# Performance work log

Measured on AMD Instinct MI355X. Metric: run time of the kernel, lower is better.

Reference implementation:

```python
import jax, jax.numpy as jnp
import numpy as np

N, M, D = 32768, 8192, 256


def setup_inputs() -> dict:
    key = jax.random.key(0)
    kx, ky = jax.random.split(key)
    inputDataX = jax.random.normal(kx, (N, D), dtype=jnp.float32)
    targetDataY = jax.random.normal(ky, (M, D), dtype=jnp.float32)
    dualVariablePsi = jnp.zeros((M,), dtype=jnp.float32)
    return {"inputDataX": inputDataX, "targetDataY": targetDataY, "dualVariablePsi": dualVariablePsi}


def reference(inputDataX, targetDataY, dualVariablePsi):
    # cost[i,j] = 0.5 * ||x_i - y_j||^2, built GEMM-style as in the torch module
    sq_x = jnp.sum(inputDataX ** 2, axis=1, keepdims=True)          # [N, 1]
    sq_y = jnp.sum(targetDataY ** 2, axis=1)[None, :]               # [1, M]
    cross = inputDataX @ targetDataY.T                              # [N, M]
    cost = (sq_x + sq_y - 2.0 * cross) * 0.5
    row_min = jnp.min(cost - dualVariablePsi[None, :], axis=1)      # [N]
    n = inputDataX.shape[0]
    return jnp.sum(row_min) / n + jnp.mean(dualVariablePsi)
```

## Files before the change

### kernel.cpp

```cpp
#include <hip/hip_runtime.h>
#include <hip/hip_bf16.h>
#include <stdint.h>

#define NROWS 32768
#define MCOLS 8192
#define DDIM  256

#define BM 128
#define BN 64
#define NT (MCOLS/BN)
#define NWG (NROWS/BM)

typedef __attribute__((ext_vector_type(8))) int   int8v;
typedef __attribute__((ext_vector_type(4))) float f32x4;

__device__ __forceinline__ uint32_t pk4_fp8(float4 v) {
  int p = __builtin_amdgcn_cvt_pk_fp8_f32(v.x, v.y, 0, false);
  p = __builtin_amdgcn_cvt_pk_fp8_f32(v.z, v.w, p, true);
  return (uint32_t)p;
}
__device__ __forceinline__ f32x4 vmin4(f32x4 x, f32x4 y) {
  f32x4 r;
  r[0] = fminf(x[0], y[0]); r[1] = fminf(x[1], y[1]);
  r[2] = fminf(x[2], y[2]); r[3] = fminf(x[3], y[3]);
  return r;
}

__global__ void k_prep(const float* __restrict__ X, const float* __restrict__ Y,
                       const float* __restrict__ psi,
                       uint32_t* __restrict__ XqN, uint32_t* __restrict__ YqT,
                       float* __restrict__ xhalf, float* __restrict__ cbuf,
                       float* __restrict__ sum_accum)
{
  const int lane = threadIdx.x & 63;
  const int gw = (blockIdx.x * blockDim.x + threadIdx.x) >> 6;
  const int nw = (gridDim.x * blockDim.x) >> 6;
  for (int row = gw; row < NROWS + MCOLS; row += nw) {
    const bool isX = row < NROWS;
    const int r = isX ? row : row - NROWS;
    const float* src = isX ? (X + (size_t)row * DDIM) : (Y + (size_t)r * DDIM);
    float4 v = ((const float4*)src)[lane];
    const uint32_t pk = pk4_fp8(v);
    if (isX) {
      XqN[(size_t)row * 64 + lane] = pk ^ 0x80808080u;
    } else {
      const int idx = (r >> 4) * 1024 + (lane >> 5) * 512 + ((lane >> 3) & 3) * 128
                    + (r & 15) * 8 + (lane & 7);
      YqT[idx] = pk;
    }
    float s = v.x*v.x + v.y*v.y + v.z*v.z + v.w*v.w;
    #pragma unroll
    for (int m = 32; m >= 1; m >>= 1) s += __shfl_xor(s, m);
    if (lane == 0) {
      if (isX) xhalf[row] = 0.5f * s;
      else     cbuf[r] = 0.5f * s - psi[r];
    }
  }
  if (blockIdx.x == 0 && threadIdx.x == 0) sum_accum[0] = 0.0f;
}

#define LOADB(dst, cjv, t_) do {                                                \
    const char* _p = bBase + (size_t)(t_) * 16384;                              \
    dst[0] = *(const int8v*)(_p);                                               \
    dst[1] = *(const int8v*)(_p + 2048);                                        \
    cjv = cjPtr[(t_) * BN];                                                     \
  } while (0)

#define STEP(t_, CUR, cjv) do {                                                 \
    const f32x4 _ci = {cjv, cjv, cjv, cjv};                                     \
    f32x4 acc[4];                                                               \
    __builtin_amdgcn_s_setprio(1);                                              \
    _Pragma("unroll") for (int _m = 0; _m < 4; ++_m)                            \
      acc[_m] = __builtin_amdgcn_mfma_scale_f32_16x16x128_f8f6f4(               \
          a[_m][0], CUR[0], _ci, 0, 0, 0, 0x7F, 0, 0x7F);                       \
    _Pragma("unroll") for (int _m = 0; _m < 4; ++_m)                            \
      acc[_m] = __builtin_amdgcn_mfma_scale_f32_16x16x128_f8f6f4(               \
          a[_m][1], CUR[1], acc[_m], 0, 0, 0, 0x7F, 0, 0x7F);                   \
    __builtin_amdgcn_s_setprio(0);                                              \
    if ((t_) + 2 < NT) LOADB(CUR, cjv, (t_) + 2);                               \
    _Pragma("unroll") for (int _m = 0; _m < 4; ++_m)                            \
      vmin[_m] = vmin4(vmin[_m], acc[_m]);                                      \
  } while (0)

__global__ __attribute__((amdgpu_flat_work_group_size(512, 512),
                          amdgpu_waves_per_eu(2, 2)))
void k_gemm(const uint32_t* __restrict__ XqN, const uint32_t* __restrict__ YqT,
            const float* __restrict__ cbuf, const float* __restrict__ xhalf,
            float* __restrict__ sum_accum)
{
  __shared__ float Rw[4][BM];
  __shared__ float part[2];

  const int brow = blockIdx.x * BM;
  const int tid  = threadIdx.x;
  const int wid  = tid >> 6;
  const int lane = tid & 63;
  const int rg    = wid >> 2;
  const int strip = wid & 3;
  const int c15 = lane & 15;
  const int w4  = lane >> 4;

  int8v a[4][2];
  {
    const char* aBase = (const char*)XqN + ((size_t)(brow + rg * 64 + c15) << 8) + w4 * 32;
    #pragma unroll
    for (int m = 0; m < 4; ++m)
      #pragma unroll
      for (int kc = 0; kc < 2; ++kc)
        a[m][kc] = *(const int8v*)(aBase + m * 4096 + kc * 128);
  }

  const char* bBase = (const char*)YqT + (size_t)strip * 4096 + (w4 * 16 + c15) * 32;
  const float* cjPtr = cbuf + strip * 16 + c15;

  int8v bA[2], bB[2];
  float cjA, cjB;
  LOADB(bA, cjA, 0);
  LOADB(bB, cjB, 1);

  f32x4 vmin[4];
  #pragma unroll
  for (int m = 0; m < 4; ++m)
    vmin[m] = (f32x4){3.4e38f, 3.4e38f, 3.4e38f, 3.4e38f};

  #pragma unroll 1
  for (int tt = 0; tt < NT; tt += 2) {
    STEP(tt,     bA, cjA);
    STEP(tt + 1, bB, cjB);
  }

  #pragma unroll
  for (int m = 0; m < 4; ++m) {
    #pragma unroll
    for (int r = 0; r < 4; ++r) {
      float v = vmin[m][r];
      v = fminf(v, __shfl_xor(v, 1));
      v = fminf(v, __shfl_xor(v, 2));
      v = fminf(v, __shfl_xor(v, 4));
      v = fminf(v, __shfl_xor(v, 8));
      vmin[m][r] = v;
    }
    if (c15 < 4) {
      float vsel = vmin[m][0];
      vsel = (c15 == 1) ? vmin[m][1] : vsel;
      vsel = (c15 == 2) ? vmin[m][2] : vsel;
      vsel = (c15 == 3) ? vmin[m][3] : vsel;
      Rw[strip][rg * 64 + m * 16 + w4 * 4 + c15] = vsel;
    }
  }
  __syncthreads();

  if (tid < BM) {
    float rm = fminf(fminf(Rw[0][tid], Rw[1][tid]),
                     fminf(Rw[2][tid], Rw[3][tid]));
    float s = rm + xhalf[brow + tid];
    #pragma unroll
    for (int m = 32; m >= 1; m >>= 1) s += __shfl_xor(s, m);
    if (lane == 0) part[wid] = s;
  }
  __syncthreads();
  if (tid == 0) atomicAdd(sum_accum, part[0] + part[1]);
}

__global__ void k_final(const float* __restrict__ psi, const float* __restrict__ sum_accum,
                        float* __restrict__ out)
{
  __shared__ float sh[4];
  float s = 0.f;
  for (int i = threadIdx.x; i < MCOLS; i += 256) s += psi[i];
  #pragma unroll
  for (int m = 32; m >= 1; m >>= 1) s += __shfl_xor(s, m);
  const int wid = threadIdx.x >> 6, lane = threadIdx.x & 63;
  if (lane == 0) sh[wid] = s;
  __syncthreads();
  if (threadIdx.x == 0)
    out[0] = sum_accum[0] / (float)NROWS + (sh[0] + sh[1] + sh[2] + sh[3]) / (float)MCOLS;
}

extern "C" void kernel_launch(void* const* d_in, const int* in_sizes, int n_in,
                              void* d_out, int out_size, void* d_ws, size_t ws_size,
                              hipStream_t stream)
{
  const float* X   = (const float*)d_in[0];
  const float* Y   = (const float*)d_in[1];
  const float* psi = (const float*)d_in[2];
  float* out = (float*)d_out;

  char* ws = (char*)d_ws;
  uint32_t* XqN    = (uint32_t*)(ws);
  uint32_t* YqT    = (uint32_t*)(ws + (size_t)NROWS * DDIM);
  float* cbuf      = (float*)(ws + (size_t)(NROWS + MCOLS) * DDIM);
  float* xhalf     = (float*)((char*)cbuf + (size_t)MCOLS * 4);
  float* sum_accum = (float*)((char*)xhalf + (size_t)NROWS * 4);

  k_prep <<<2048, 256, 0, stream>>>(X, Y, psi, XqN, YqT, xhalf, cbuf, sum_accum);
  k_gemm <<<NWG, 512, 0, stream>>>(XqN, YqT, cbuf, xhalf, sum_accum);
  k_final<<<1, 256, 0, stream>>>(psi, sum_accum, out);
}
```

Baseline: 79.93 us.

## Split GEMM columns across two workgroups with atomicMin row keys

Each row block's column sweep is now split in half across two workgroups, doubling the grid to 512 workgroups, and waves_per_eu is relaxed to allow higher occupancy. Partial row minima are merged with an atomicMin on an order-preserving integer encoding of the float. A new reduction kernel then adds xhalf and sums the rows. The aim is to fill the GPU better, since 256 workgroups underfill the compute units. The cost is an extra kernel launch, global atomics, and the A-fragment loads being repeated in both halves.

```diff
diff --git a/kernel.cpp b/kernel.cpp
--- a/kernel.cpp
+++ b/kernel.cpp
@@ -8,8 +8,8 @@
 
 #define BM 128
 #define BN 64
-#define NT (MCOLS/BN)
-#define NWG (NROWS/BM)
+#define NT 64
+#define NWG 512
 
 typedef __attribute__((ext_vector_type(8))) int   int8v;
 typedef __attribute__((ext_vector_type(4))) float f32x4;
@@ -18,6 +18,14 @@
   int p = __builtin_amdgcn_cvt_pk_fp8_f32(v.x, v.y, 0, false);
   p = __builtin_amdgcn_cvt_pk_fp8_f32(v.z, v.w, p, true);
   return (uint32_t)p;
+}
+__device__ __forceinline__ uint32_t fkey(float f) {
+  uint32_t b = __float_as_uint(f);
+  return (b & 0x80000000u) ? ~b : (b | 0x80000000u);
+}
+__device__ __forceinline__ float funkey(uint32_t k) {
+  uint32_t b = (k & 0x80000000u) ? (k ^ 0x80000000u) : ~k;
+  return __uint_as_float(b);
 }
 __device__ __forceinline__ f32x4 vmin4(f32x4 x, f32x4 y) {
   f32x4 r;
@@ -30,7 +38,7 @@
                        const float* __restrict__ psi,
                        uint32_t* __restrict__ XqN, uint32_t* __restrict__ YqT,
                        float* __restrict__ xhalf, float* __restrict__ cbuf,
-                       float* __restrict__ sum_accum)
+                       uint32_t* __restrict__ rowkey, float* __restrict__ sum_accum)
 {
   const int lane = threadIdx.x & 63;
   const int gw = (blockIdx.x * blockDim.x + threadIdx.x) >> 6;
@@ -52,8 +60,8 @@
     #pragma unroll
     for (int m = 32; m >= 1; m >>= 1) s += __shfl_xor(s, m);
     if (lane == 0) {
-      if (isX) xhalf[row] = 0.5f * s;
-      else     cbuf[r] = 0.5f * s - psi[r];
+      if (isX) { xhalf[row] = 0.5f * s; rowkey[row] = 0xFFFFFFFFu; }
+      else     { cbuf[r] = 0.5f * s - psi[r]; }
     }
   }
   if (blockIdx.x == 0 && threadIdx.x == 0) sum_accum[0] = 0.0f;
@@ -83,15 +91,14 @@
   } while (0)
 
 __global__ __attribute__((amdgpu_flat_work_group_size(512, 512),
-                          amdgpu_waves_per_eu(2, 2)))
+                          amdgpu_waves_per_eu(2, 4)))
 void k_gemm(const uint32_t* __restrict__ XqN, const uint32_t* __restrict__ YqT,
-            const float* __restrict__ cbuf, const float* __restrict__ xhalf,
-            float* __restrict__ sum_accum)
+            const float* __restrict__ cbuf, uint32_t* __restrict__ rowkey)
 {
   __shared__ float Rw[4][BM];
-  __shared__ float part[2];
-
-  const int brow = blockIdx.x * BM;
+
+  const int brow = (blockIdx.x >> 1) * BM;
+  const int bcol = (blockIdx.x & 1) * (MCOLS / 2);
   const int tid  = threadIdx.x;
   const int wid  = tid >> 6;
   const int lane = tid & 63;
@@ -110,8 +117,9 @@
         a[m][kc] = *(const int8v*)(aBase + m * 4096 + kc * 128);
   }
 
-  const char* bBase = (const char*)YqT + (size_t)strip * 4096 + (w4 * 16 + c15) * 32;
-  const float* cjPtr = cbuf + strip * 16 + c15;
+  const char* bBase = (const char*)YqT + (size_t)(bcol >> 6) * 16384
+                      + (size_t)strip * 4096 + (w4 * 16 + c15) * 32;
+  const float* cjPtr = cbuf + bcol + strip * 16 + c15;
 
   int8v bA[2], bB[2];
   float cjA, cjB;
@@ -153,13 +161,22 @@
   if (tid < BM) {
     float rm = fminf(fminf(Rw[0][tid], Rw[1][tid]),
                      fminf(Rw[2][tid], Rw[3][tid]));
-    float s = rm + xhalf[brow + tid];
-    #pragma unroll
-    for (int m = 32; m >= 1; m >>= 1) s += __shfl_xor(s, m);
-    if (lane == 0) part[wid] = s;
-  }
+    atomicMin((unsigned int*)&rowkey[brow + tid], fkey(rm));
+  }
+}
+
+__global__ void k_rowred(const float* __restrict__ xhalf, const uint32_t* __restrict__ rowkey,
+                         float* __restrict__ sum_accum)
+{
+  __shared__ float sh[4];
+  const int i = blockIdx.x * 256 + threadIdx.x;
+  float v = funkey(rowkey[i]) + xhalf[i];
+  #pragma unroll
+  for (int m = 32; m >= 1; m >>= 1) v += __shfl_xor(v, m);
+  const int wid = threadIdx.x >> 6, lane = threadIdx.x & 63;
+  if (lane == 0) sh[wid] = v;
   __syncthreads();
-  if (tid == 0) atomicAdd(sum_accum, part[0] + part[1]);
+  if (threadIdx.x == 0) atomicAdd(sum_accum, sh[0] + sh[1] + sh[2] + sh[3]);
 }
 
 __global__ void k_final(const float* __restrict__ psi, const float* __restrict__ sum_accum,
@@ -190,10 +207,12 @@
   uint32_t* XqN    = (uint32_t*)(ws);
   uint32_t* YqT    = (uint32_t*)(ws + (size_t)NROWS * DDIM);
   float* cbuf      = (float*)(ws + (size_t)(NROWS + MCOLS) * DDIM);
-  float* xhalf     = (float*)((char*)cbuf + (size_t)MCOLS * 4);
+  uint32_t* rowkey = (uint32_t*)((char*)cbuf + (size_t)MCOLS * 4);
+  float* xhalf     = (float*)((char*)rowkey + (size_t)NROWS * 4);
   float* sum_accum = (float*)((char*)xhalf + (size_t)NROWS * 4);
 
-  k_prep <<<2048, 256, 0, stream>>>(X, Y, psi, XqN, YqT, xhalf, cbuf, sum_accum);
-  k_gemm <<<NWG, 512, 0, stream>>>(XqN, YqT, cbuf, xhalf, sum_accum);
-  k_final<<<1, 256, 0, stream>>>(psi, sum_accum, out);
-}
+  k_prep  <<<2048, 256, 0, stream>>>(X, Y, psi, XqN, YqT, xhalf, cbuf, rowkey, sum_accum);
+  k_gemm  <<<NWG, 512, 0, stream>>>(XqN, YqT, cbuf, rowkey);
+  k_rowred<<<NROWS / 256, 256, 0, stream>>>(xhalf, rowkey, sum_accum);
+  k_final <<<1, 256, 0, stream>>>(psi, sum_accum, out);
+}
```

Measured after the change: 86.13 us. 7.8% more time.
